# Kernel optimization log

Hardware: AMD Instinct MI355X
Metric: run time of the kernel (lower is better)

Reference implementation:

```python
import jax, jax.numpy as jnp
import numpy as np


def setup_inputs() -> dict:
    key = jax.random.key(0)
    ks = jax.random.split(key, 12)
    B = 131072
    s = lambda fan_in: 1.0 / np.sqrt(fan_in)
    inp = {
        "x": jax.random.normal(ks[0], (B, 2, 13, 21), dtype=jnp.float32),
        # depthwise 3x3, groups=2, no bias: OIHW with O=2, I=1
        "dw_w": jax.random.uniform(ks[1], (2, 1, 3, 3), jnp.float32, -s(9), s(9)),
        # pointwise 1x1: 2 -> 5
        "pw_w": jax.random.uniform(ks[2], (5, 2, 1, 1), jnp.float32, -s(2), s(2)),
        "pw_b": jax.random.uniform(ks[3], (5,), jnp.float32, -s(2), s(2)),
        # conv 1x1: 5 -> 5
        "conv_w": jax.random.uniform(ks[4], (5, 5, 1, 1), jnp.float32, -s(5), s(5)),
        "conv_b": jax.random.uniform(ks[5], (5,), jnp.float32, -s(5), s(5)),
        # dense 90 -> 16 -> 16 -> 14 (torch Linear layout: [out, in])
        "w1": jax.random.uniform(ks[6], (16, 90), jnp.float32, -s(90), s(90)),
        "b1": jax.random.uniform(ks[7], (16,), jnp.float32, -s(90), s(90)),
        "w2": jax.random.uniform(ks[8], (16, 16), jnp.float32, -s(16), s(16)),
        "b2": jax.random.uniform(ks[9], (16,), jnp.float32, -s(16), s(16)),
        "w3": jax.random.uniform(ks[10], (14, 16), jnp.float32, -s(16), s(16)),
        "b3": jax.random.uniform(ks[11], (14,), jnp.float32, -s(16), s(16)),
    }
    return inp


def _conv(x, w, groups=1):
    return jax.lax.conv_general_dilated(
        x, w, window_strides=(1, 1), padding="VALID",
        dimension_numbers=("NCHW", "OIHW", "NCHW"),
        feature_group_count=groups)


def reference(x, dw_w, pw_w, pw_b, conv_w, conv_b, w1, b1, w2, b2, w3, b3):
    # depthwise-separable conv: depthwise 3x3 (groups=2, no bias) + pointwise 1x1
    h = _conv(x, dw_w, groups=2)                      # [B,2,11,19]
    h = _conv(h, pw_w) + pw_b[None, :, None, None]    # [B,5,11,19]
    h = jnp.tanh(h)
    h = _conv(h, conv_w) + conv_b[None, :, None, None]  # 1x1 conv 5->5
    h = jnp.tanh(h)
    # AvgPool2d(3): kernel=stride=3, no padding -> crop to 9x18, reshape-mean
    h = h[:, :, :9, :18]
    B = h.shape[0]
    h = h.reshape(B, 5, 3, 3, 6, 3).mean(axis=(3, 5))  # [B,5,3,6]
    h = jnp.tanh(h)
    h = h.reshape(B, 90)
    h = jnp.tanh(h @ w1.T + b1)
    h = jnp.tanh(h @ w2.T + b2)
    return h @ w3.T + b3                               # [B,14]
```

## Files before the change

kernel.cpp:

```cpp
#include <hip/hip_runtime.h>

typedef float f4v __attribute__((ext_vector_type(4), aligned(4)));
typedef float f2v __attribute__((ext_vector_type(2), aligned(8)));

__device__ __forceinline__ float fast_tanh(float x) {
  float t = x * 2.8853900817779268f;
#if __has_builtin(__builtin_amdgcn_exp2f)
  float e = __builtin_amdgcn_exp2f(t);
#else
  float e = exp2f(t);
#endif
#if __has_builtin(__builtin_amdgcn_rcpf)
  float r = __builtin_amdgcn_rcpf(e + 1.0f);
#else
  float r = 1.0f / (e + 1.0f);
#endif
  return 1.0f - 2.0f * r;
}

__device__ __forceinline__ void loadrow(const float* __restrict__ xs, int row,
                                        float* __restrict__ d0,
                                        float* __restrict__ d1) {
  const f4v* p0 = reinterpret_cast<const f4v*>(xs + row * 21);
  const f4v* p1 = reinterpret_cast<const f4v*>(xs + 273 + row * 21);
#pragma unroll
  for (int k = 0; k < 5; ++k) {
    f4v a = p0[k];
    f4v b = p1[k];
#pragma unroll
    for (int l = 0; l < 4; ++l) {
      d0[4 * k + l] = a[l];
      d1[4 * k + l] = b[l];
    }
  }
}

__global__ __launch_bounds__(256, 2) void smartpixel_kernel(
    const float* __restrict__ x, const float* __restrict__ dw_w,
    const float* __restrict__ pw_w, const float* __restrict__ pw_b,
    const float* __restrict__ conv_w, const float* __restrict__ conv_b,
    const float* __restrict__ w1, const float* __restrict__ b1,
    const float* __restrict__ w2, const float* __restrict__ b2,
    const float* __restrict__ w3, const float* __restrict__ b3,
    float* __restrict__ out, int nsamp) {
  const int s = blockIdx.x * 256 + threadIdx.x;
  if (s >= nsamp) return;
  const float* xs = x + (long)s * 546;

  float w0r[3][20], w1r[3][20];
  float pf0[20], pf1[20];

  loadrow(xs, 0, w0r[1], w1r[1]);
  loadrow(xs, 1, w0r[2], w1r[2]);
  loadrow(xs, 2, pf0, pf1);

  float pool[5][6];
#pragma unroll
  for (int c = 0; c < 5; ++c)
#pragma unroll
    for (int j = 0; j < 6; ++j) pool[c][j] = 0.0f;

  float h1a[16];
#pragma unroll
  for (int o = 0; o < 16; ++o) h1a[o] = b1[o];

#pragma unroll 1
  for (int i = 0; i < 9; ++i) {
#pragma unroll
    for (int k = 0; k < 20; ++k) {
      w0r[0][k] = w0r[1][k]; w0r[1][k] = w0r[2][k]; w0r[2][k] = pf0[k];
      w1r[0][k] = w1r[1][k]; w1r[1][k] = w1r[2][k]; w1r[2][k] = pf1[k];
    }
    int lr = i + 3; if (lr > 10) lr = 10;
    loadrow(xs, lr, pf0, pf1);

#pragma unroll
    for (int j = 0; j < 18; ++j) {
      float d0 = w0r[0][j] * dw_w[0] + w0r[0][j + 1] * dw_w[1] + w0r[0][j + 2] * dw_w[2]
               + w0r[1][j] * dw_w[3] + w0r[1][j + 1] * dw_w[4] + w0r[1][j + 2] * dw_w[5]
               + w0r[2][j] * dw_w[6] + w0r[2][j + 1] * dw_w[7] + w0r[2][j + 2] * dw_w[8];
      float d1 = w1r[0][j] * dw_w[9]  + w1r[0][j + 1] * dw_w[10] + w1r[0][j + 2] * dw_w[11]
               + w1r[1][j] * dw_w[12] + w1r[1][j + 1] * dw_w[13] + w1r[1][j + 2] * dw_w[14]
               + w1r[2][j] * dw_w[15] + w1r[2][j + 1] * dw_w[16] + w1r[2][j + 2] * dw_w[17];
      float aa[5];
#pragma unroll
      for (int p = 0; p < 5; ++p)
        aa[p] = fast_tanh(pw_b[p] + pw_w[2 * p] * d0 + pw_w[2 * p + 1] * d1);
#pragma unroll
      for (int q = 0; q < 5; ++q) {
        float acc = conv_b[q];
#pragma unroll
        for (int p = 0; p < 5; ++p) acc += conv_w[5 * q + p] * aa[p];
        pool[q][j / 3] += fast_tanh(acc);
      }
    }

    if ((i % 3) == 2) {
      int rr = i / 3;
#pragma unroll
      for (int c = 0; c < 5; ++c)
#pragma unroll
        for (int j = 0; j < 6; ++j) {
          float pc = fast_tanh(pool[c][j] * (1.0f / 9.0f));
          pool[c][j] = 0.0f;
          int fidx = c * 18 + rr * 6 + j;
#pragma unroll
          for (int o = 0; o < 16; ++o) h1a[o] += pc * w1[o * 90 + fidx];
        }
    }
  }

  float h1[16];
#pragma unroll
  for (int k = 0; k < 16; ++k) h1[k] = fast_tanh(h1a[k]);
  float h2[16];
#pragma unroll
  for (int o = 0; o < 16; ++o) {
    float acc = b2[o];
#pragma unroll
    for (int k = 0; k < 16; ++k) acc += h1[k] * w2[o * 16 + k];
    h2[o] = fast_tanh(acc);
  }
  float ov[14];
#pragma unroll
  for (int o = 0; o < 14; ++o) {
    float acc = b3[o];
#pragma unroll
    for (int k = 0; k < 16; ++k) acc += h2[k] * w3[o * 16 + k];
    ov[o] = acc;
  }
  f2v* po = reinterpret_cast<f2v*>(out + (long)s * 14);
#pragma unroll
  for (int k = 0; k < 7; ++k) {
    f2v v;
    v[0] = ov[2 * k];
    v[1] = ov[2 * k + 1];
    po[k] = v;
  }
}

extern "C" void kernel_launch(void* const* d_in, const int* in_sizes, int n_in,
                              void* d_out, int out_size, void* d_ws, size_t ws_size,
                              hipStream_t stream) {
  const float* x      = (const float*)d_in[0];
  const float* dw_w   = (const float*)d_in[1];
  const float* pw_w   = (const float*)d_in[2];
  const float* pw_b   = (const float*)d_in[3];
  const float* conv_w = (const float*)d_in[4];
  const float* conv_b = (const float*)d_in[5];
  const float* w1     = (const float*)d_in[6];
  const float* b1     = (const float*)d_in[7];
  const float* w2     = (const float*)d_in[8];
  const float* b2     = (const float*)d_in[9];
  const float* w3     = (const float*)d_in[10];
  const float* b3     = (const float*)d_in[11];
  float* out = (float*)d_out;

  int nsamp = in_sizes[0] / 546;
  int blocks = (nsamp + 255) / 256;
  smartpixel_kernel<<<blocks, 256, 0, stream>>>(
      x, dw_w, pw_w, pw_b, conv_w, conv_b, w1, b1, w2, b2, w3, b3, out, nsamp);
}
```

Before: 115.0 us.

## Split each sample across two threads by column halves with shuffle reduction

Each sample is now processed by two adjacent lanes, each covering 9 of the 18 conv output columns. The layer-1 partial sums are combined with a lane shuffle, and each lane writes 7 of the 14 outputs. The rolling row buffer is replaced by a 4-slot register ring that is statically rotated through templated row bodies, and occupancy is raised to 3 blocks. This doubles the number of threads and cuts per-thread register pressure and serial latency. The cost is a duplicated layer-2 MLP and more thread launches.

```diff
diff --git a/kernel.cpp b/kernel.cpp
--- a/kernel.cpp
+++ b/kernel.cpp
@@ -1,118 +1,127 @@
 #include <hip/hip_runtime.h>
 
 typedef float f4v __attribute__((ext_vector_type(4), aligned(4)));
-typedef float f2v __attribute__((ext_vector_type(2), aligned(8)));
+typedef float f2v __attribute__((ext_vector_type(2), aligned(4)));
 
 __device__ __forceinline__ float fast_tanh(float x) {
   float t = x * 2.8853900817779268f;
-#if __has_builtin(__builtin_amdgcn_exp2f)
   float e = __builtin_amdgcn_exp2f(t);
-#else
-  float e = exp2f(t);
-#endif
-#if __has_builtin(__builtin_amdgcn_rcpf)
   float r = __builtin_amdgcn_rcpf(e + 1.0f);
-#else
-  float r = 1.0f / (e + 1.0f);
-#endif
   return 1.0f - 2.0f * r;
 }
 
-__device__ __forceinline__ void loadrow(const float* __restrict__ xs, int row,
-                                        float* __restrict__ d0,
-                                        float* __restrict__ d1) {
-  const f4v* p0 = reinterpret_cast<const f4v*>(xs + row * 21);
-  const f4v* p1 = reinterpret_cast<const f4v*>(xs + 273 + row * 21);
+__device__ __forceinline__ void ldrow(const float* __restrict__ base, int rowoff,
+                                      float (&d0)[12], float (&d1)[12]) {
 #pragma unroll
-  for (int k = 0; k < 5; ++k) {
-    f4v a = p0[k];
-    f4v b = p1[k];
+  for (int kk = 0; kk < 3; ++kk) {
+    f4v a = *reinterpret_cast<const f4v*>(base + rowoff * 21 + 4 * kk);
+    f4v b = *reinterpret_cast<const f4v*>(base + 273 + rowoff * 21 + 4 * kk);
 #pragma unroll
     for (int l = 0; l < 4; ++l) {
-      d0[4 * k + l] = a[l];
-      d1[4 * k + l] = b[l];
+      d0[4 * kk + l] = a[l];
+      d1[4 * kk + l] = b[l];
     }
   }
 }
 
-__global__ __launch_bounds__(256, 2) void smartpixel_kernel(
-    const float* __restrict__ x, const float* __restrict__ dw_w,
-    const float* __restrict__ pw_w, const float* __restrict__ pw_b,
-    const float* __restrict__ conv_w, const float* __restrict__ conv_b,
+template <int S0, int S1, int S2>
+__device__ __forceinline__ void row_body(
+    const float (&W0)[4][12], const float (&W1)[4][12],
+    const float* __restrict__ dww, const float* __restrict__ pww,
+    const float* __restrict__ pwb, const float* __restrict__ cvw,
+    const float* __restrict__ cvb, float (&pool)[5][3]) {
+#pragma unroll
+  for (int j = 0; j < 9; ++j) {
+    float d0 = W0[S0][j] * dww[0] + W0[S0][j + 1] * dww[1] + W0[S0][j + 2] * dww[2]
+             + W0[S1][j] * dww[3] + W0[S1][j + 1] * dww[4] + W0[S1][j + 2] * dww[5]
+             + W0[S2][j] * dww[6] + W0[S2][j + 1] * dww[7] + W0[S2][j + 2] * dww[8];
+    float d1 = W1[S0][j] * dww[9]  + W1[S0][j + 1] * dww[10] + W1[S0][j + 2] * dww[11]
+             + W1[S1][j] * dww[12] + W1[S1][j + 1] * dww[13] + W1[S1][j + 2] * dww[14]
+             + W1[S2][j] * dww[15] + W1[S2][j + 1] * dww[16] + W1[S2][j + 2] * dww[17];
+    float aa[5];
+#pragma unroll
+    for (int p = 0; p < 5; ++p)
+      aa[p] = fast_tanh(pwb[p] + pww[2 * p] * d0 + pww[2 * p + 1] * d1);
+#pragma unroll
+    for (int q = 0; q < 5; ++q) {
+      float acc = cvb[q];
+#pragma unroll
+      for (int p = 0; p < 5; ++p) acc += cvw[5 * q + p] * aa[p];
+      pool[q][j / 3] += fast_tanh(acc);
+    }
+  }
+}
+
+template <int RR>
+__device__ __forceinline__ void pool_finish(float (&pool)[5][3], float (&h1a)[16],
+                                            const float* __restrict__ w1t) {
+#pragma unroll
+  for (int c = 0; c < 5; ++c)
+#pragma unroll
+    for (int pc = 0; pc < 3; ++pc) {
+      float pv = fast_tanh(pool[c][pc] * (1.0f / 9.0f));
+      pool[c][pc] = 0.0f;
+#pragma unroll
+      for (int o = 0; o < 16; ++o)
+        h1a[o] += pv * w1t[o * 90 + c * 18 + RR * 6 + pc];
+    }
+}
+
+__global__ __launch_bounds__(256, 3) void smartpixel_kernel(
+    const float* __restrict__ x, const float* __restrict__ dww,
+    const float* __restrict__ pww, const float* __restrict__ pwb,
+    const float* __restrict__ cvw, const float* __restrict__ cvb,
     const float* __restrict__ w1, const float* __restrict__ b1,
     const float* __restrict__ w2, const float* __restrict__ b2,
     const float* __restrict__ w3, const float* __restrict__ b3,
     float* __restrict__ out, int nsamp) {
-  const int s = blockIdx.x * 256 + threadIdx.x;
+  const int g = blockIdx.x * 256 + threadIdx.x;
+  const int s = g >> 1;
+  const int t = g & 1;
   if (s >= nsamp) return;
-  const float* xs = x + (long)s * 546;
+  const float* xb = x + (long)s * 546 + t * 9;
 
-  float w0r[3][20], w1r[3][20];
-  float pf0[20], pf1[20];
+  float W0[4][12], W1[4][12];
+  ldrow(xb, 0, W0[0], W1[0]);
+  ldrow(xb, 1, W0[1], W1[1]);
+  ldrow(xb, 2, W0[2], W1[2]);
 
-  loadrow(xs, 0, w0r[1], w1r[1]);
-  loadrow(xs, 1, w0r[2], w1r[2]);
-  loadrow(xs, 2, pf0, pf1);
-
-  float pool[5][6];
+  float pool[5][3];
 #pragma unroll
   for (int c = 0; c < 5; ++c)
 #pragma unroll
-    for (int j = 0; j < 6; ++j) pool[c][j] = 0.0f;
+    for (int pc = 0; pc < 3; ++pc) pool[c][pc] = 0.0f;
 
   float h1a[16];
 #pragma unroll
-  for (int o = 0; o < 16; ++o) h1a[o] = b1[o];
+  for (int o = 0; o < 16; ++o) h1a[o] = (t == 0) ? b1[o] : 0.0f;
+
+  const float* w1t = w1 + 3 * t;
 
 #pragma unroll 1
-  for (int i = 0; i < 9; ++i) {
-#pragma unroll
-    for (int k = 0; k < 20; ++k) {
-      w0r[0][k] = w0r[1][k]; w0r[1][k] = w0r[2][k]; w0r[2][k] = pf0[k];
-      w1r[0][k] = w1r[1][k]; w1r[1][k] = w1r[2][k]; w1r[2][k] = pf1[k];
-    }
-    int lr = i + 3; if (lr > 10) lr = 10;
-    loadrow(xs, lr, pf0, pf1);
+  for (int ig = 0; ig < 2; ++ig) {
+    const float* xr = xb + ig * 84;
+    ldrow(xr, 3, W0[3], W1[3]);
+    row_body<0, 1, 2>(W0, W1, dww, pww, pwb, cvw, cvb, pool);
+    ldrow(xr, 4, W0[0], W1[0]);
+    row_body<1, 2, 3>(W0, W1, dww, pww, pwb, cvw, cvb, pool);
+    if (ig == 1) pool_finish<1>(pool, h1a, w1t);
+    ldrow(xr, 5, W0[1], W1[1]);
+    row_body<2, 3, 0>(W0, W1, dww, pww, pwb, cvw, cvb, pool);
+    if (ig == 0) pool_finish<0>(pool, h1a, w1t);
+    ldrow(xr, 6, W0[2], W1[2]);
+    row_body<3, 0, 1>(W0, W1, dww, pww, pwb, cvw, cvb, pool);
+  }
+  row_body<0, 1, 2>(W0, W1, dww, pww, pwb, cvw, cvb, pool);
+  pool_finish<2>(pool, h1a, w1t);
 
 #pragma unroll
-    for (int j = 0; j < 18; ++j) {
-      float d0 = w0r[0][j] * dw_w[0] + w0r[0][j + 1] * dw_w[1] + w0r[0][j + 2] * dw_w[2]
-               + w0r[1][j] * dw_w[3] + w0r[1][j + 1] * dw_w[4] + w0r[1][j + 2] * dw_w[5]
-               + w0r[2][j] * dw_w[6] + w0r[2][j + 1] * dw_w[7] + w0r[2][j + 2] * dw_w[8];
-      float d1 = w1r[0][j] * dw_w[9]  + w1r[0][j + 1] * dw_w[10] + w1r[0][j + 2] * dw_w[11]
-               + w1r[1][j] * dw_w[12] + w1r[1][j + 1] * dw_w[13] + w1r[1][j + 2] * dw_w[14]
-               + w1r[2][j] * dw_w[15] + w1r[2][j + 1] * dw_w[16] + w1r[2][j + 2] * dw_w[17];
-      float aa[5];
-#pragma unroll
-      for (int p = 0; p < 5; ++p)
-        aa[p] = fast_tanh(pw_b[p] + pw_w[2 * p] * d0 + pw_w[2 * p + 1] * d1);
-#pragma unroll
-      for (int q = 0; q < 5; ++q) {
-        float acc = conv_b[q];
-#pragma unroll
-        for (int p = 0; p < 5; ++p) acc += conv_w[5 * q + p] * aa[p];
-        pool[q][j / 3] += fast_tanh(acc);
-      }
-    }
-
-    if ((i % 3) == 2) {
-      int rr = i / 3;
-#pragma unroll
-      for (int c = 0; c < 5; ++c)
-#pragma unroll
-        for (int j = 0; j < 6; ++j) {
-          float pc = fast_tanh(pool[c][j] * (1.0f / 9.0f));
-          pool[c][j] = 0.0f;
-          int fidx = c * 18 + rr * 6 + j;
-#pragma unroll
-          for (int o = 0; o < 16; ++o) h1a[o] += pc * w1[o * 90 + fidx];
-        }
-    }
-  }
+  for (int o = 0; o < 16; ++o) h1a[o] += __shfl_xor(h1a[o], 1, 64);
 
   float h1[16];
 #pragma unroll
   for (int k = 0; k < 16; ++k) h1[k] = fast_tanh(h1a[k]);
+
   float h2[16];
 #pragma unroll
   for (int o = 0; o < 16; ++o) {
@@ -121,22 +130,22 @@
     for (int k = 0; k < 16; ++k) acc += h1[k] * w2[o * 16 + k];
     h2[o] = fast_tanh(acc);
   }
-  float ov[14];
+
+  const int ob = 7 * t;
+  float ov[7];
 #pragma unroll
-  for (int o = 0; o < 14; ++o) {
-    float acc = b3[o];
+  for (int oo = 0; oo < 7; ++oo) {
+    float acc = b3[ob + oo];
 #pragma unroll
-    for (int k = 0; k < 16; ++k) acc += h2[k] * w3[o * 16 + k];
-    ov[o] = acc;
+    for (int k = 0; k < 16; ++k) acc += h2[k] * w3[(ob + oo) * 16 + k];
+    ov[oo] = acc;
   }
-  f2v* po = reinterpret_cast<f2v*>(out + (long)s * 14);
-#pragma unroll
-  for (int k = 0; k < 7; ++k) {
-    f2v v;
-    v[0] = ov[2 * k];
-    v[1] = ov[2 * k + 1];
-    po[k] = v;
-  }
+  float* po = out + (long)s * 14 + ob;
+  f4v v4; v4[0] = ov[0]; v4[1] = ov[1]; v4[2] = ov[2]; v4[3] = ov[3];
+  *reinterpret_cast<f4v*>(po) = v4;
+  f2v v2; v2[0] = ov[4]; v2[1] = ov[5];
+  *reinterpret_cast<f2v*>(po + 4) = v2;
+  po[6] = ov[6];
 }
 
 extern "C" void kernel_launch(void* const* d_in, const int* in_sizes, int n_in,
@@ -157,7 +166,8 @@
   float* out = (float*)d_out;
 
   int nsamp = in_sizes[0] / 546;
-  int blocks = (nsamp + 255) / 256;
+  long nthreads = 2L * nsamp;
+  int blocks = (int)((nthreads + 255) / 256);
   smartpixel_kernel<<<blocks, 256, 0, stream>>>(
       x, dw_w, pw_w, pw_b, conv_w, conv_b, w1, b1, w2, b2, w3, b3, out, nsamp);
 }
```

Result: slower. 255.9 us (+122.6%).
